# Kernel optimization log

Hardware: AMD Instinct MI355X
Metric: run time of the kernel (lower is better)

## Reference

```python
import jax, jax.numpy as jnp
import numpy as np

N, L, E, H = 4, 2048, 512, 8
D = E // H


def setup_inputs() -> dict:
    key = jax.random.key(0)
    ks = jax.random.split(key, 8)
    causal = jnp.tril(jnp.ones((L, L), dtype=bool))[None, None]  # [1,1,L,L]
    return {
        "values": jax.random.normal(ks[0], (N, L, E), dtype=jnp.float32),
        "keys": jax.random.normal(ks[1], (N, L, E), dtype=jnp.float32),
        "query": jax.random.normal(ks[2], (N, L, E), dtype=jnp.float32),
        "mask": causal,
        "Wv": jax.random.normal(ks[3], (D, D), dtype=jnp.float32) * 0.05,
        "Wk": jax.random.normal(ks[4], (D, D), dtype=jnp.float32) * 0.05,
        "Wq": jax.random.normal(ks[5], (D, D), dtype=jnp.float32) * 0.05,
        "Wo": jax.random.normal(ks[6], (E, E), dtype=jnp.float32) * 0.05,
        "bo": jnp.zeros((E,), dtype=jnp.float32),
    }


def reference(values, keys, query, mask, Wv, Wk, Wq, Wo, bo):
    n, ql, e = query.shape
    # split heads: [N, len, H, D]
    v = values.reshape(n, -1, H, D)
    k = keys.reshape(n, -1, H, D)
    q = query.reshape(n, ql, H, D)
    # per-head linear projections (nn.Linear: x @ W.T, no bias)
    v = jnp.einsum("nlhd,od->nlho", v, Wv)
    k = jnp.einsum("nlhd,od->nlho", k, Wk)
    q = jnp.einsum("nqhd,od->nqho", q, Wq)
    # scores [N, H, Q, K]
    energy = jnp.einsum("nqhd,nkhd->nhqk", q, k)
    energy = jnp.where(mask == 0, jnp.float32(-1e28), energy)
    # NOTE: module scales by embed_size**0.5, not head_dim**0.5 (faithful)
    attn = jax.nn.softmax(energy / np.float32(e ** 0.5), axis=3)
    out = jnp.einsum("nhqk,nkhd->nqhd", attn, v).reshape(n, ql, e)
    return out @ Wo.T + bo
```

## Files before the change

kernel.cpp:

```cpp
#include <hip/hip_runtime.h>

#define NB 4
#define LL 2048
#define EE 512
#define HH 8
#define DD 64

typedef __attribute__((ext_vector_type(8))) short short8;
typedef __attribute__((ext_vector_type(4))) float f32x4;
typedef __attribute__((ext_vector_type(16))) float f32x16;
typedef __attribute__((ext_vector_type(4))) unsigned int u32x4;
typedef __attribute__((ext_vector_type(2))) int i32x2;
typedef __bf16 bf16x8 __attribute__((ext_vector_type(8)));

#if __has_builtin(__builtin_amdgcn_exp2f)
#define EXP2(x) __builtin_amdgcn_exp2f(x)
#else
#define EXP2(x) __expf((x) * 0.6931471805599453f)
#endif

#define QSCALE (0.04419417382415922f * 1.4426950408889634f)
#define MSHIFT 4.0f

static __device__ __forceinline__ short bfc(float f) {
    return __builtin_bit_cast(short, (__bf16)f);
}

static __device__ __forceinline__ unsigned pkbf(float lo, float hi) {
    unsigned short a = (unsigned short)(unsigned)__builtin_bit_cast(unsigned short, (__bf16)lo);
    unsigned short b = (unsigned short)(unsigned)__builtin_bit_cast(unsigned short, (__bf16)hi);
    return (unsigned)a | ((unsigned)b << 16);
}

static __device__ __forceinline__ f32x4 mfma16(short8 a, short8 b, f32x4 c) {
    return __builtin_amdgcn_mfma_f32_16x16x32_bf16(
        __builtin_bit_cast(bf16x8, a), __builtin_bit_cast(bf16x8, b), c, 0, 0, 0);
}

static __device__ __forceinline__ f32x16 mfma32(short8 a, short8 b, f32x16 c) {
    return __builtin_amdgcn_mfma_f32_32x32x16_bf16(
        __builtin_bit_cast(bf16x8, a), __builtin_bit_cast(bf16x8, b), c, 0, 0, 0);
}

__global__ __launch_bounds__(256, 4) void k_proj(const float* __restrict__ vals,
                                                 const float* __restrict__ keys,
                                                 const float* __restrict__ qry,
                                                 const float* __restrict__ Wv,
                                                 const float* __restrict__ Wk,
                                                 const float* __restrict__ Wq,
                                                 const float* __restrict__ Wo,
                                                 unsigned short* __restrict__ Qp,
                                                 unsigned short* __restrict__ Kp,
                                                 unsigned short* __restrict__ Vg,
                                                 unsigned short* __restrict__ Wob) {
    __shared__ __align__(16) unsigned short smem[16512];

    const int tid = threadIdx.x;
    const int w = tid >> 6, ln = tid & 63;
    const int c = ln & 15, g = ln >> 4;

    if (blockIdx.x < 512) {
        {
            const int i = blockIdx.x * 512 + tid * 2;
            float2 v = *(const float2*)(Wo + i);
            Wob[i] = (unsigned short)bfc(v.x);
            Wob[i + 1] = (unsigned short)bfc(v.y);
        }
        unsigned short (*kq)[8256] = (unsigned short (*)[8256])smem;
        const int r0 = blockIdx.x * 128;
        const int n = r0 >> 14;
        const int l0 = (r0 >> 3) & (LL - 1);
        const int h = c & 7;

#pragma unroll
        for (int t = 0; t < 2; ++t) {
            const float* X = t ? qry : keys;
            const float* W = t ? Wq : Wk;

            short8 xf[2][2];
#pragma unroll
            for (int rt = 0; rt < 2; ++rt) {
                const int r = r0 + w * 32 + rt * 16 + c;
#pragma unroll
                for (int kk = 0; kk < 2; ++kk) {
                    const float* p = X + (size_t)r * DD + kk * 32 + g * 8;
                    short8 v;
#pragma unroll
                    for (int j = 0; j < 8; ++j) v[j] = bfc(p[j]);
                    xf[rt][kk] = v;
                }
            }
            short8 wf[4][2];
#pragma unroll
            for (int nt = 0; nt < 4; ++nt)
#pragma unroll
                for (int kk = 0; kk < 2; ++kk) {
                    const float* p = W + (nt * 16 + c) * DD + kk * 32 + g * 8;
                    short8 v;
#pragma unroll
                    for (int j = 0; j < 8; ++j) v[j] = bfc(p[j]);
                    wf[nt][kk] = v;
                }

#pragma unroll
            for (int rt = 0; rt < 2; ++rt) {
                const int l15 = w * 4 + rt * 2 + (c >> 3);
#pragma unroll
                for (int nt = 0; nt < 4; ++nt) {
                    f32x4 acc = {0.f, 0.f, 0.f, 0.f};
                    acc = mfma16(wf[nt][0], xf[rt][0], acc);
                    acc = mfma16(wf[nt][1], xf[rt][1], acc);
                    const int o = nt * 16 + g * 4;
                    const float s = t ? QSCALE : 1.0f;
                    uint2 u = {pkbf(acc[0] * s, acc[1] * s), pkbf(acc[2] * s, acc[3] * s)};
                    *(uint2*)&kq[t][h * 1032 + l15 * 64 + o] = u;
                }
            }
        }
        __syncthreads();

#pragma unroll
        for (int t = 0; t < 2; ++t) {
            unsigned short* dstb = t ? Qp : Kp;
            const int hh = tid >> 5, s = tid & 31;
#pragma unroll
            for (int i = 0; i < 4; ++i) {
                const int q = s * 4 + i;
                const int l = q >> 3, cc = q & 7;
                uint4 v = *(const uint4*)&kq[t][hh * 1032 + l * 64 + cc * 8];
                *(uint4*)(dstb + ((size_t)(n * HH + hh) * LL + l0 + l) * DD + cc * 8) = v;
            }
        }
    } else {
        unsigned short* vv = smem;
        const int r0 = (blockIdx.x - 512) * 128;
        const int n = r0 >> 14;
        const int l0 = (r0 >> 3) & (LL - 1);
        const int h = c & 7;

        short8 xf[2][2];
#pragma unroll
        for (int rt = 0; rt < 2; ++rt) {
            const int r = r0 + w * 32 + rt * 16 + c;
#pragma unroll
            for (int kk = 0; kk < 2; ++kk) {
                const float* p = vals + (size_t)r * DD + kk * 32 + g * 8;
                short8 v;
#pragma unroll
                for (int j = 0; j < 8; ++j) v[j] = bfc(p[j]);
                xf[rt][kk] = v;
            }
        }
        short8 wf[4][2];
#pragma unroll
        for (int nt = 0; nt < 4; ++nt)
#pragma unroll
            for (int kk = 0; kk < 2; ++kk) {
                const float* p = Wv + (nt * 16 + c) * DD + kk * 32 + g * 8;
                short8 v;
#pragma unroll
                for (int j = 0; j < 8; ++j) v[j] = bfc(p[j]);
                wf[nt][kk] = v;
            }

#pragma unroll
        for (int rt = 0; rt < 2; ++rt) {
            const int l15 = w * 4 + rt * 2 + (c >> 3);
#pragma unroll
            for (int nt = 0; nt < 4; ++nt) {
                f32x4 acc = {0.f, 0.f, 0.f, 0.f};
                acc = mfma16(wf[nt][0], xf[rt][0], acc);
                acc = mfma16(wf[nt][1], xf[rt][1], acc);
                const int o = nt * 16 + g * 4;
#pragma unroll
                for (int reg = 0; reg < 4; ++reg)
                    vv[h * 1284 + (o + reg) * 20 + l15] = (unsigned short)bfc(acc[reg]);
            }
        }
        __syncthreads();

#pragma unroll
        for (int pi = 0; pi < 2; ++pi) {
            const int p = tid + pi * 256;
            const int hh = p >> 6, d = p & 63;
            const unsigned short* sp = &vv[hh * 1284 + d * 20];
            uint2 r0v = *(const uint2*)(sp + 0);
            uint2 r1v = *(const uint2*)(sp + 4);
            uint2 r2v = *(const uint2*)(sp + 8);
            uint2 r3v = *(const uint2*)(sp + 12);
            u32x4 o0 = {r0v.x, r0v.y, r1v.x, r1v.y};
            u32x4 o1 = {r2v.x, r2v.y, r3v.x, r3v.y};
            unsigned short* dst = Vg + (size_t)(n * HH + hh) * (LL * DD) +
                                  (size_t)(l0 >> 4) * 1024 + d * 16;
            *(u32x4*)dst = o0;
            *(u32x4*)(dst + 8) = o1;
        }
    }
}

static __device__ __forceinline__ void stage_tile(const unsigned short* __restrict__ src,
                                                  unsigned short* buf, int w, int ln,
                                                  size_t rstride) {
#pragma unroll
    for (int r = 0; r < 2; ++r) {
        int qi = w * 2 + r;
        int row = qi * 8 + (ln >> 3);
        int s = (ln & 7) ^ (row & 7);
        __builtin_amdgcn_global_load_lds(
            (const __attribute__((address_space(1))) unsigned int*)(src + (size_t)row * rstride + s * 8),
            (__attribute__((address_space(3))) unsigned int*)(buf + qi * 512),
            16, 0, 0);
    }
}

static __device__ __forceinline__ void stage_v(const unsigned short* __restrict__ src,
                                               unsigned short* buf, int w, int ln) {
#pragma unroll
    for (int r = 0; r < 2; ++r) {
        int idx = w * 64 + ln + r * 256;
        int d = idx >> 3, c16 = idx & 7;
        int cc = c16 ^ (d & 7);
        __builtin_amdgcn_global_load_lds(
            (const __attribute__((address_space(1))) unsigned int*)(src + (cc >> 1) * 1024 + d * 16 + (cc & 1) * 8),
            (__attribute__((address_space(3))) unsigned int*)(buf + idx * 8),
            16, 0, 0);
    }
}

__global__ __launch_bounds__(256, 4) void k_attn(const unsigned short* __restrict__ Qp,
                                                 const unsigned short* __restrict__ Kp,
                                                 const unsigned short* __restrict__ Vg,
                                                 unsigned short* __restrict__ Xa) {
    __shared__ __align__(16) unsigned short Kt[2][64 * 64];
    __shared__ __align__(16) unsigned short Vt[2][64 * 64];

    const int tid = threadIdx.x;
    const int w = tid >> 6, ln = tid & 63;
    const int c31 = ln & 31, g2 = ln >> 5;
    const int qpair = w >> 1, kvh = w & 1;

    const int b = blockIdx.x;
    const int x8 = b & 7;
    const int idx = b >> 3;
    const int nh = (x8 << 2) | (idx & 3);
    const int jj = (idx >> 2) & 15;
    const int j = (idx >> 6) ? jj : 31 - jj;
    const int qt = 2 * j + qpair;
    const int Q0 = qt * 32;
    const int nIter = j + 1;

    const unsigned short* Qb = Qp + (size_t)nh * (LL * DD);
    const unsigned short* Kb = Kp + (size_t)nh * (LL * DD);
    const unsigned short* Vb = Vg + (size_t)nh * (LL * DD);

    short8 qf[4];
#pragma unroll
    for (int kc = 0; kc < 4; ++kc)
        qf[kc] = *(const short8*)(Qb + (Q0 + c31) * DD + kc * 16 + g2 * 8);

    f32x16 oacc0, oacc1;
#pragma unroll
    for (int r = 0; r < 16; ++r) { oacc0[r] = 0.f; oacc1[r] = 0.f; }
    float lsum = 0.f;

    stage_tile(Kb, &Kt[0][0], w, ln, DD);
    stage_v(Vb, &Vt[0][0], w, ln);
    __syncthreads();

    int cur = 0;
    for (int t = 0; t < nIter; ++t) {
        const int nxt = cur ^ 1;
        if (t + 1 < nIter) {
            stage_tile(Kb + (size_t)(t + 1) * (64 * DD), &Kt[nxt][0], w, ln, DD);
            stage_v(Vb + (size_t)(t + 1) * 4096, &Vt[nxt][0], w, ln);
        }

        const int kb32 = t * 64 + kvh * 32;
        if (kb32 <= Q0 + 31) {
            const char* kb_ = (const char*)&Kt[cur][0];
            const char* vb_ = (const char*)&Vt[cur][0];
            const int q = Q0 + c31;

            f32x16 sc;
#pragma unroll
            for (int r = 0; r < 16; ++r) sc[r] = -MSHIFT;
            {
                const int R = kvh * 32 + c31;
                const unsigned rb = (unsigned)(R * 128);
                const unsigned swz = (unsigned)((R & 7) << 4);
                __builtin_amdgcn_s_setprio(1);
#pragma unroll
                for (int kc = 0; kc < 4; ++kc) {
                    short8 af = *(const short8*)(kb_ + rb + (((unsigned)(kc * 32 + g2 * 16)) ^ swz));
                    sc = mfma32(af, qf[kc], sc);
                }
                __builtin_amdgcn_s_setprio(0);
            }

            if (kb32 + 31 > Q0) {
#pragma unroll
                for (int r = 0; r < 16; ++r) {
                    int kvg = kb32 + (r & 3) + 8 * (r >> 2) + 4 * g2;
                    sc[r] = (kvg > q) ? -1e30f : sc[r];
                }
            }

#pragma unroll
            for (int r = 0; r < 16; ++r) sc[r] = EXP2(sc[r]);
            {
                float a[8];
#pragma unroll
                for (int r = 0; r < 8; ++r) a[r] = sc[r] + sc[r + 8];
                float b0 = a[0] + a[4], b1 = a[1] + a[5];
                float b2 = a[2] + a[6], b3 = a[3] + a[7];
                lsum += (b0 + b1) + (b2 + b3);
            }

            unsigned pk[8];
#pragma unroll
            for (int iw = 0; iw < 8; ++iw) pk[iw] = pkbf(sc[2 * iw], sc[2 * iw + 1]);
#pragma unroll
            for (int ck = 0; ck < 2; ++ck) {
                unsigned s0 = g2 ? pk[4 * ck + 0] : pk[4 * ck + 2];
                unsigned s1 = g2 ? pk[4 * ck + 1] : pk[4 * ck + 3];
                unsigned x0 = __shfl_xor(s0, 32);
                unsigned x1 = __shfl_xor(s1, 32);
                u32x4 bfv;
                bfv[0] = g2 ? x0 : pk[4 * ck + 0];
                bfv[1] = g2 ? x1 : pk[4 * ck + 1];
                bfv[2] = g2 ? pk[4 * ck + 2] : x0;
                bfv[3] = g2 ? pk[4 * ck + 3] : x1;
                short8 pB = __builtin_bit_cast(short8, bfv);
                const unsigned coff = (unsigned)(kvh * 64 + ck * 32 + g2 * 16);
                __builtin_amdgcn_s_setprio(1);
                {
                    const int dP = c31;
                    short8 A = *(const short8*)(vb_ + (unsigned)(dP * 128) +
                                                (coff ^ ((unsigned)((dP & 7) << 4))));
                    oacc0 = mfma32(A, pB, oacc0);
                }
                {
                    const int dP = 32 + c31;
                    short8 A = *(const short8*)(vb_ + (unsigned)(dP * 128) +
                                                (coff ^ ((unsigned)((dP & 7) << 4))));
                    oacc1 = mfma32(A, pB, oacc1);
                }
                __builtin_amdgcn_s_setprio(0);
            }
        }

        __syncthreads();
        cur = nxt;
    }

    {
        float* lb = (float*)(&Kt[0][0]);
        float* ob = (float*)(&Vt[0][0]);
        if (kvh) {
            float* op = ob + qpair * 2048;
#pragma unroll
            for (int r = 0; r < 16; ++r) {
                op[r * 64 + ln] = oacc0[r];
                op[(16 + r) * 64 + ln] = oacc1[r];
            }
            lb[qpair * 64 + ln] = lsum;
        }
        __syncthreads();
        if (kvh) return;
        {
            const float* op = ob + qpair * 2048;
#pragma unroll
            for (int r = 0; r < 16; ++r) {
                oacc0[r] += op[r * 64 + ln];
                oacc1[r] += op[(16 + r) * 64 + ln];
            }
            lsum += lb[qpair * 64 + ln];
        }
    }

    lsum += __shfl_xor(lsum, 32);
    const float inv = 1.0f / lsum;
    const int n = nh >> 3, h = nh & 7;
    unsigned short* orow = Xa + ((size_t)(n * LL + Q0 + c31)) * EE + h * DD;
#pragma unroll
    for (int a = 0; a < 4; ++a) {
        {
            float e0 = oacc0[4 * a + 0] * inv, e1 = oacc0[4 * a + 1] * inv;
            float e2 = oacc0[4 * a + 2] * inv, e3 = oacc0[4 * a + 3] * inv;
            uint2 u = {pkbf(e0, e1), pkbf(e2, e3)};
            *(uint2*)(orow + a * 8 + g2 * 4) = u;
        }
        {
            float e0 = oacc1[4 * a + 0] * inv, e1 = oacc1[4 * a + 1] * inv;
            float e2 = oacc1[4 * a + 2] * inv, e3 = oacc1[4 * a + 3] * inv;
            uint2 u = {pkbf(e0, e1), pkbf(e2, e3)};
            *(uint2*)(orow + 32 + a * 8 + g2 * 4) = u;
        }
    }
}

__global__ __launch_bounds__(256) void k_out(const unsigned short* __restrict__ X,
                                             const unsigned short* __restrict__ Wob,
                                             const float* __restrict__ bo,
                                             float* __restrict__ out) {
    const int tid = threadIdx.x, w = tid >> 6, ln = tid & 63, c = ln & 15, g = ln >> 4;
    const int b = blockIdx.x;
    const int x8 = b & 7, jj = b >> 3;
    const int mb = x8 * 8 + (jj & 7);
    const int nb = jj >> 3;
    const int mbase = mb * 128 + w * 16;
    const int nbase = nb * 64;

    const unsigned short* Xr0 = X + (size_t)(mbase + c) * EE + g * 8;
    const unsigned short* Xr1 = X + (size_t)(mbase + 64 + c) * EE + g * 8;
    const unsigned short* Wr = Wob + (size_t)(nbase + c) * EE + g * 8;

    f32x4 acc0[4] = {}, acc1[4] = {};
    short8 a0 = *(const short8*)(Xr0);
    short8 a1 = *(const short8*)(Xr1);
    short8 bf[4];
#pragma unroll
    for (int nt = 0; nt < 4; ++nt) bf[nt] = *(const short8*)(Wr + (size_t)nt * 16 * EE);

#pragma unroll
    for (int ks = 0; ks < 16; ++ks) {
        short8 na0, na1, nbf[4];
        if (ks < 15) {
            na0 = *(const short8*)(Xr0 + (ks + 1) * 32);
            na1 = *(const short8*)(Xr1 + (ks + 1) * 32);
#pragma unroll
            for (int nt = 0; nt < 4; ++nt)
                nbf[nt] = *(const short8*)(Wr + (size_t)nt * 16 * EE + (ks + 1) * 32);
        }
#pragma unroll
        for (int nt = 0; nt < 4; ++nt) {
            acc0[nt] = mfma16(a0, bf[nt], acc0[nt]);
            acc1[nt] = mfma16(a1, bf[nt], acc1[nt]);
        }
        if (ks < 15) {
            a0 = na0; a1 = na1;
#pragma unroll
            for (int nt = 0; nt < 4; ++nt) bf[nt] = nbf[nt];
        }
    }
#pragma unroll
    for (int nt = 0; nt < 4; ++nt) {
        float bias = bo[nbase + nt * 16 + c];
#pragma unroll
        for (int reg = 0; reg < 4; ++reg) {
            int row0 = mbase + g * 4 + reg;
            out[(size_t)row0 * EE + nbase + nt * 16 + c] = acc0[nt][reg] + bias;
            out[(size_t)(row0 + 64) * EE + nbase + nt * 16 + c] = acc1[nt][reg] + bias;
        }
    }
}

extern "C" void kernel_launch(void* const* d_in, const int* in_sizes, int n_in,
                              void* d_out, int out_size, void* d_ws, size_t ws_size,
                              hipStream_t stream) {
    const float* vals = (const float*)d_in[0];
    const float* keys = (const float*)d_in[1];
    const float* qry  = (const float*)d_in[2];
    const float* Wv = (const float*)d_in[4];
    const float* Wk = (const float*)d_in[5];
    const float* Wq = (const float*)d_in[6];
    const float* Wo = (const float*)d_in[7];
    const float* bo = (const float*)d_in[8];
    float* out = (float*)d_out;

    char* ws = (char*)d_ws;
    unsigned short* Qp  = (unsigned short*)(ws);
    unsigned short* Kp  = (unsigned short*)(ws + (8u  << 20));
    unsigned short* Vg  = (unsigned short*)(ws + (16u << 20));
    unsigned short* Xa  = (unsigned short*)(ws + (24u << 20));
    unsigned short* Wob = (unsigned short*)(ws + (32u << 20));

    hipLaunchKernelGGL(k_proj, dim3(1024), dim3(256), 0, stream,
                       vals, keys, qry, Wv, Wk, Wq, Wo, Qp, Kp, Vg, Wob);
    hipLaunchKernelGGL(k_attn, dim3(1024), dim3(256), 0, stream, Qp, Kp, Vg, Xa);
    hipLaunchKernelGGL(k_out, dim3(512), dim3(256), 0, stream, Xa, Wob, bo, out);
}
```

Measured before the change: 89.31 us.

## Widen attention blocks to 512 threads sharing K/V tiles across four query tiles

The attention kernel now uses 8 waves per block covering four 32-row query tiles instead of two, so each staged 64-row K/V tile is reused by twice as many waves. The grid drops from 1024 to 512 blocks, and each thread issues one async global-to-LDS load per tile instead of two. The cross-wave reduction buffers move from aliased K/V LDS into dedicated shared arrays. The aim is to halve redundant K/V global traffic and staging work. In exchange, per-block LDS grows and there are fewer, larger blocks. Under the causal mask more waves also sit idle on tiles past their diagonal, which can hurt load balance and occupancy.

```diff
diff --git a/kernel.cpp b/kernel.cpp
--- a/kernel.cpp
+++ b/kernel.cpp
@@ -198,41 +198,35 @@
     }
 }
 
-static __device__ __forceinline__ void stage_tile(const unsigned short* __restrict__ src,
-                                                  unsigned short* buf, int w, int ln,
-                                                  size_t rstride) {
-#pragma unroll
-    for (int r = 0; r < 2; ++r) {
-        int qi = w * 2 + r;
-        int row = qi * 8 + (ln >> 3);
-        int s = (ln & 7) ^ (row & 7);
-        __builtin_amdgcn_global_load_lds(
-            (const __attribute__((address_space(1))) unsigned int*)(src + (size_t)row * rstride + s * 8),
-            (__attribute__((address_space(3))) unsigned int*)(buf + qi * 512),
-            16, 0, 0);
-    }
-}
-
-static __device__ __forceinline__ void stage_v(const unsigned short* __restrict__ src,
-                                               unsigned short* buf, int w, int ln) {
-#pragma unroll
-    for (int r = 0; r < 2; ++r) {
-        int idx = w * 64 + ln + r * 256;
-        int d = idx >> 3, c16 = idx & 7;
-        int cc = c16 ^ (d & 7);
-        __builtin_amdgcn_global_load_lds(
-            (const __attribute__((address_space(1))) unsigned int*)(src + (cc >> 1) * 1024 + d * 16 + (cc & 1) * 8),
-            (__attribute__((address_space(3))) unsigned int*)(buf + idx * 8),
-            16, 0, 0);
-    }
-}
-
-__global__ __launch_bounds__(256, 4) void k_attn(const unsigned short* __restrict__ Qp,
+static __device__ __forceinline__ void stage_tile512(const unsigned short* __restrict__ src,
+                                                     unsigned short* buf, int tid,
+                                                     size_t rstride) {
+    int row = tid >> 3;
+    int s = (tid & 7) ^ (row & 7);
+    __builtin_amdgcn_global_load_lds(
+        (const __attribute__((address_space(1))) unsigned int*)(src + (size_t)row * rstride + s * 8),
+        (__attribute__((address_space(3))) unsigned int*)(buf + tid * 8),
+        16, 0, 0);
+}
+
+static __device__ __forceinline__ void stage_v512(const unsigned short* __restrict__ src,
+                                                  unsigned short* buf, int tid) {
+    int d = tid >> 3, c16 = tid & 7;
+    int cc = c16 ^ (d & 7);
+    __builtin_amdgcn_global_load_lds(
+        (const __attribute__((address_space(1))) unsigned int*)(src + (cc >> 1) * 1024 + d * 16 + (cc & 1) * 8),
+        (__attribute__((address_space(3))) unsigned int*)(buf + tid * 8),
+        16, 0, 0);
+    }
+
+__global__ __launch_bounds__(512, 4) void k_attn(const unsigned short* __restrict__ Qp,
                                                  const unsigned short* __restrict__ Kp,
                                                  const unsigned short* __restrict__ Vg,
                                                  unsigned short* __restrict__ Xa) {
     __shared__ __align__(16) unsigned short Kt[2][64 * 64];
     __shared__ __align__(16) unsigned short Vt[2][64 * 64];
+    __shared__ __align__(16) float ob[4][32][64];
+    __shared__ float lb[4][64];
 
     const int tid = threadIdx.x;
     const int w = tid >> 6, ln = tid & 63;
@@ -243,11 +237,11 @@
     const int x8 = b & 7;
     const int idx = b >> 3;
     const int nh = (x8 << 2) | (idx & 3);
-    const int jj = (idx >> 2) & 15;
-    const int j = (idx >> 6) ? jj : 31 - jj;
-    const int qt = 2 * j + qpair;
+    const int qq = (idx >> 2) & 7;
+    const int j = (idx >> 5) ? qq : 15 - qq;
+    const int qt = 4 * j + qpair;
     const int Q0 = qt * 32;
-    const int nIter = j + 1;
+    const int nIter = 2 * j + 2;
 
     const unsigned short* Qb = Qp + (size_t)nh * (LL * DD);
     const unsigned short* Kb = Kp + (size_t)nh * (LL * DD);
@@ -263,16 +257,16 @@
     for (int r = 0; r < 16; ++r) { oacc0[r] = 0.f; oacc1[r] = 0.f; }
     float lsum = 0.f;
 
-    stage_tile(Kb, &Kt[0][0], w, ln, DD);
-    stage_v(Vb, &Vt[0][0], w, ln);
+    stage_tile512(Kb, &Kt[0][0], tid, DD);
+    stage_v512(Vb, &Vt[0][0], tid);
     __syncthreads();
 
     int cur = 0;
     for (int t = 0; t < nIter; ++t) {
         const int nxt = cur ^ 1;
         if (t + 1 < nIter) {
-            stage_tile(Kb + (size_t)(t + 1) * (64 * DD), &Kt[nxt][0], w, ln, DD);
-            stage_v(Vb + (size_t)(t + 1) * 4096, &Vt[nxt][0], w, ln);
+            stage_tile512(Kb + (size_t)(t + 1) * (64 * DD), &Kt[nxt][0], tid, DD);
+            stage_v512(Vb + (size_t)(t + 1) * 4096, &Vt[nxt][0], tid);
         }
 
         const int kb32 = t * 64 + kvh * 32;
@@ -353,30 +347,22 @@
         cur = nxt;
     }
 
-    {
-        float* lb = (float*)(&Kt[0][0]);
-        float* ob = (float*)(&Vt[0][0]);
-        if (kvh) {
-            float* op = ob + qpair * 2048;
-#pragma unroll
-            for (int r = 0; r < 16; ++r) {
-                op[r * 64 + ln] = oacc0[r];
-                op[(16 + r) * 64 + ln] = oacc1[r];
-            }
-            lb[qpair * 64 + ln] = lsum;
-        }
-        __syncthreads();
-        if (kvh) return;
-        {
-            const float* op = ob + qpair * 2048;
-#pragma unroll
-            for (int r = 0; r < 16; ++r) {
-                oacc0[r] += op[r * 64 + ln];
-                oacc1[r] += op[(16 + r) * 64 + ln];
-            }
-            lsum += lb[qpair * 64 + ln];
-        }
-    }
+    if (kvh) {
+#pragma unroll
+        for (int r = 0; r < 16; ++r) {
+            ob[qpair][r][ln] = oacc0[r];
+            ob[qpair][16 + r][ln] = oacc1[r];
+        }
+        lb[qpair][ln] = lsum;
+    }
+    __syncthreads();
+    if (kvh) return;
+#pragma unroll
+    for (int r = 0; r < 16; ++r) {
+        oacc0[r] += ob[qpair][r][ln];
+        oacc1[r] += ob[qpair][16 + r][ln];
+    }
+    lsum += lb[qpair][ln];
 
     lsum += __shfl_xor(lsum, 32);
     const float inv = 1.0f / lsum;
@@ -477,6 +463,6 @@
 
     hipLaunchKernelGGL(k_proj, dim3(1024), dim3(256), 0, stream,
                        vals, keys, qry, Wv, Wk, Wq, Wo, Qp, Kp, Vg, Wob);
-    hipLaunchKernelGGL(k_attn, dim3(1024), dim3(256), 0, stream, Qp, Kp, Vg, Xa);
+    hipLaunchKernelGGL(k_attn, dim3(512), dim3(512), 0, stream, Qp, Kp, Vg, Xa);
     hipLaunchKernelGGL(k_out, dim3(512), dim3(256), 0, stream, Xa, Wob, bo, out);
 }
```

Measured after the change: 93.63 us. 1.05x slower.
